# Kernel optimization log

Hardware: AMD Instinct MI355X
Metric: run time of the kernel (lower is better)

The kernel has to match this reference:

```python
import jax, jax.numpy as jnp
import numpy as np

BITS = 32
HDC_DIM = 512
IN_SCALE = 23  # 1 + 2*input_window_size, window=11


def setup_inputs() -> dict:
    key = jax.random.key(0)
    k1, k2, k3, k4 = jax.random.split(key, 4)
    B = 2
    D = IN_SCALE * IN_SCALE  # 529
    num_nonzero = int(0.5 * D * HDC_DIM)  # 135424
    return {
        "data_input": jax.random.normal(k1, (B, 4 * IN_SCALE, IN_SCALE), dtype=jnp.float32),
        "structure_input": jax.random.normal(k2, (B, IN_SCALE, IN_SCALE), dtype=jnp.float32),
        "parameters_temp": jax.random.uniform(k3, (IN_SCALE, IN_SCALE), dtype=jnp.float32),
        "non_zero_indices": jax.random.randint(k4, (num_nonzero,), 0, D * HDC_DIM, dtype=jnp.int32),
    }


def _bit_unpack(x_float):
    # view float32 bits as int32, unpack into 0/1 per bit (little-endian bit order),
    # matching torch: x.unsqueeze(-1).bitwise_and(2**arange(bits)).ne(0)
    xi = jax.lax.bitcast_convert_type(x_float, jnp.int32)
    mask = jnp.left_shift(jnp.int32(1), jnp.arange(BITS, dtype=jnp.int32))  # [32], incl. sign bit
    return ((xi[..., None] & mask) != 0).astype(jnp.int32)  # [..., 32]


def reference(data_input, structure_input, parameters_temp, non_zero_indices):
    B = data_input.shape[0]
    n = IN_SCALE
    # channel slices
    r = data_input[:, 0:n, :].reshape(B, -1)            # [B, D]
    g = data_input[:, n:2 * n, :].reshape(B, -1)
    b = data_input[:, 2 * n:3 * n, :].reshape(B, -1)
    a = data_input[:, 3 * n:4 * n, :].reshape(B, -1)
    s = (structure_input * parameters_temp).reshape(B, -1)  # [B, D]
    D = r.shape[1]

    # sparse random scatter into flat projection buffer (faithful to torch semantics:
    # view(-1)[idx] = 1, then view(-1)[~idx] = 0 where ~idx indexes total-1-idx via negative wrap)
    total = B * D * BITS * HDC_DIM
    proj = jnp.zeros((total,), dtype=jnp.int32)
    proj = proj.at[non_zero_indices].set(1)
    proj = proj.at[total - 1 - non_zero_indices].set(0)
    proj = proj.reshape(B, D, BITS, HDC_DIM)

    # bit-unpack + broadcast-XOR against projection (no materialized repeat)
    r_bin = _bit_unpack(r)[..., None] ^ proj  # [B, D, 32, hdc]
    g_bin = _bit_unpack(g)[..., None] ^ proj
    b_bin = _bit_unpack(b)[..., None] ^ proj
    a_bin = _bit_unpack(a)[..., None] ^ proj
    s_bin = _bit_unpack(s)[..., None] ^ proj

    return (r, g, b, a, s, r_bin, g_bin, b_bin, a_bin, s_bin)
```

## Files before the change

kernel.cpp:

```cpp
#include <hip/hip_runtime.h>
#include <stdint.h>

#define DDIM 529
#define BATCH 2
#define BITS 32
#define HDC 512
#define ROW (BITS * HDC)
#define NNZ_REGION (DDIM * HDC)
#define SMALL (5 * BATCH * DDIM)
#define BIN_PER_OUT (BATCH * DDIM * ROW)
#define TOTAL_FLOATS (SMALL + 5 * BIN_PER_OUT)
#define Q_BEG 1323
#define Q_END (TOTAL_FLOATS / 4)

typedef float f32x4 __attribute__((ext_vector_type(4)));

__device__ __forceinline__ unsigned rowword(int r,
                                            const float* __restrict__ data,
                                            const float* __restrict__ structure,
                                            const float* __restrict__ params) {
    int c   = r / (BATCH * DDIM);
    int rem = r - c * (BATCH * DDIM);
    int bb  = rem / DDIM;
    int d   = rem - bb * DDIM;
    float v = (c < 4) ? data[bb * (4 * DDIM) + c * DDIM + d]
                      : structure[bb * DDIM + d] * params[d];
    return (unsigned)__float_as_int(v);
}

__global__ __launch_bounds__(256) void stream4(const float* __restrict__ data,
                                               const float* __restrict__ structure,
                                               const float* __restrict__ params,
                                               float* __restrict__ out) {
    const unsigned nt = gridDim.x * 256u;
    f32x4* o4 = (f32x4*)out;
    for (unsigned q = Q_BEG + blockIdx.x * 256u + threadIdx.x; q < Q_END; q += nt) {
        unsigned E0 = 4u * q - SMALL;
        unsigned E2 = E0 + 2u;
        int r0 = (int)(E0 >> 14);
        int r2 = (int)(E2 >> 14);
        unsigned w0 = rowword(r0, data, structure, params);
        unsigned w2 = (r2 == r0) ? w0 : rowword(r2, data, structure, params);
        float fa = (float)((w0 >> ((E0 & 16383u) >> 9)) & 1u);
        float fb = (float)((w2 >> ((E2 & 16383u) >> 9)) & 1u);
        f32x4 v = {fa, fa, fb, fb};
        o4[q] = v;
    }
}

__global__ __launch_bounds__(256) void finalize(const int* __restrict__ idx, int n,
                                                const float* __restrict__ data,
                                                const float* __restrict__ structure,
                                                const float* __restrict__ params,
                                                float* __restrict__ out) {
    int i = blockIdx.x * blockDim.x + threadIdx.x;

    if (i < SMALL) {
        unsigned w = rowword(i, data, structure, params);
        out[i] = __int_as_float((int)w);
        if (i == 0) {
            float f = (float)(w & 1u);
            out[SMALL] = f; out[SMALL + 1] = f;
        }
        if (i == SMALL - 1) {
            float f = (float)(w >> 31);
            out[TOTAL_FLOATS - 2] = f; out[TOTAL_FLOATS - 1] = f;
        }
    }

    if (i < n) {
        unsigned p = (unsigned)idx[i];
        if (p < NNZ_REGION) {
            unsigned d = p >> 14;
            unsigned j = (p >> 9) & 31u;
            #pragma unroll
            for (int c = 0; c < 5; ++c) {
                float v = (c < 4) ? data[c * DDIM + d] : structure[d] * params[d];
                unsigned bit = ((unsigned)__float_as_int(v) >> j) & 1u;
                out[(size_t)SMALL + (size_t)c * BIN_PER_OUT + p] = (float)(bit ^ 1u);
            }
        }
    }
}

extern "C" void kernel_launch(void* const* d_in, const int* in_sizes, int n_in,
                              void* d_out, int out_size, void* d_ws, size_t ws_size,
                              hipStream_t stream) {
    const float* data      = (const float*)d_in[0];
    const float* structure = (const float*)d_in[1];
    const float* params    = (const float*)d_in[2];
    const int*   nzi       = (const int*)d_in[3];
    int nnz = in_sizes[3];

    float* out = (float*)d_out;

    stream4<<<2048, 256, 0, stream>>>(data, structure, params, out);
    finalize<<<(nnz + 255) / 256, 256, 0, stream>>>(nzi, nnz, data, structure, params, out);
}
```

Baseline: 83.81 us.

## Give each block a contiguous chunk and cache row words in shared memory

The streaming kernel now assigns each block a contiguous range of output quads instead of a grid-stride loop. The few source words that range needs are computed once into shared memory, which removes per-element global loads and integer divisions. The small-output writes and boundary fixups move from the finalize kernel into this prologue. The contiguous chunks give a different memory access pattern and add a block-wide barrier, and the hand-tuned chunk constants must exactly cover the output range.

Result: faster. 77.31 us (median of 2 runs) (-7.8%).

```diff
diff --git a/kernel.cpp b/kernel.cpp
--- a/kernel.cpp
+++ b/kernel.cpp
@@ -5,13 +5,14 @@
 #define BATCH 2
 #define BITS 32
 #define HDC 512
-#define ROW (BITS * HDC)
 #define NNZ_REGION (DDIM * HDC)
 #define SMALL (5 * BATCH * DDIM)
-#define BIN_PER_OUT (BATCH * DDIM * ROW)
+#define BIN_PER_OUT (BATCH * DDIM * 16384)
 #define TOTAL_FLOATS (SMALL + 5 * BIN_PER_OUT)
-#define Q_BEG 1323
+#define Q0 1328
 #define Q_END (TOTAL_FLOATS / 4)
+#define LQ 10584
+#define NBLK 2048
 
 typedef float f32x4 __attribute__((ext_vector_type(4)));
 
@@ -32,17 +33,39 @@
                                                const float* __restrict__ structure,
                                                const float* __restrict__ params,
                                                float* __restrict__ out) {
-    const unsigned nt = gridDim.x * 256u;
+    __shared__ int wds[4];
+    const unsigned qa = Q0 + blockIdx.x * LQ;
+    const unsigned qe = min(qa + LQ, (unsigned)Q_END);
+    const int r_lo = (int)((4u * qa - SMALL) >> 14);
+    const int t = threadIdx.x;
+    if (t < 4) {
+        int r = r_lo + t;
+        unsigned w = 0u;
+        if (r < SMALL) {
+            w = rowword(r, data, structure, params);
+            out[r] = __int_as_float((int)w);
+        }
+        wds[t] = (int)w;
+    } else if (blockIdx.x == 0) {
+        if (t >= 32 && t < 54) {
+            unsigned w0 = rowword(0, data, structure, params);
+            out[SMALL + (t - 32)] = (float)(w0 & 1u);
+        } else if (t == 54) {
+            unsigned w = rowword(SMALL - 1, data, structure, params);
+            float f = (float)(w >> 31);
+            out[TOTAL_FLOATS - 2] = f; out[TOTAL_FLOATS - 1] = f;
+        }
+    }
+    __syncthreads();
+
     f32x4* o4 = (f32x4*)out;
-    for (unsigned q = Q_BEG + blockIdx.x * 256u + threadIdx.x; q < Q_END; q += nt) {
+    for (unsigned q = qa + t; q < qe; q += 256u) {
         unsigned E0 = 4u * q - SMALL;
         unsigned E2 = E0 + 2u;
-        int r0 = (int)(E0 >> 14);
-        int r2 = (int)(E2 >> 14);
-        unsigned w0 = rowword(r0, data, structure, params);
-        unsigned w2 = (r2 == r0) ? w0 : rowword(r2, data, structure, params);
+        unsigned w0 = (unsigned)wds[(E0 >> 14) - r_lo];
+        unsigned w1 = (unsigned)wds[(E2 >> 14) - r_lo];
         float fa = (float)((w0 >> ((E0 & 16383u) >> 9)) & 1u);
-        float fb = (float)((w2 >> ((E2 & 16383u) >> 9)) & 1u);
+        float fb = (float)((w1 >> ((E2 & 16383u) >> 9)) & 1u);
         f32x4 v = {fa, fa, fb, fb};
         o4[q] = v;
     }
@@ -54,32 +77,16 @@
                                                 const float* __restrict__ params,
                                                 float* __restrict__ out) {
     int i = blockIdx.x * blockDim.x + threadIdx.x;
-
-    if (i < SMALL) {
-        unsigned w = rowword(i, data, structure, params);
-        out[i] = __int_as_float((int)w);
-        if (i == 0) {
-            float f = (float)(w & 1u);
-            out[SMALL] = f; out[SMALL + 1] = f;
-        }
-        if (i == SMALL - 1) {
-            float f = (float)(w >> 31);
-            out[TOTAL_FLOATS - 2] = f; out[TOTAL_FLOATS - 1] = f;
-        }
-    }
-
-    if (i < n) {
-        unsigned p = (unsigned)idx[i];
-        if (p < NNZ_REGION) {
-            unsigned d = p >> 14;
-            unsigned j = (p >> 9) & 31u;
-            #pragma unroll
-            for (int c = 0; c < 5; ++c) {
-                float v = (c < 4) ? data[c * DDIM + d] : structure[d] * params[d];
-                unsigned bit = ((unsigned)__float_as_int(v) >> j) & 1u;
-                out[(size_t)SMALL + (size_t)c * BIN_PER_OUT + p] = (float)(bit ^ 1u);
-            }
-        }
+    if (i >= n) return;
+    unsigned p = (unsigned)idx[i];
+    if (p >= NNZ_REGION) return;
+    unsigned d = p >> 14;
+    unsigned j = (p >> 9) & 31u;
+    #pragma unroll
+    for (int c = 0; c < 5; ++c) {
+        float v = (c < 4) ? data[c * DDIM + d] : structure[d] * params[d];
+        unsigned bit = ((unsigned)__float_as_int(v) >> j) & 1u;
+        out[(size_t)SMALL + (size_t)c * BIN_PER_OUT + p] = (float)(bit ^ 1u);
     }
 }
 
@@ -94,6 +101,6 @@
 
     float* out = (float*)d_out;
 
-    stream4<<<2048, 256, 0, stream>>>(data, structure, params, out);
+    stream4<<<NBLK, 256, 0, stream>>>(data, structure, params, out);
     finalize<<<(nnz + 255) / 256, 256, 0, stream>>>(nzi, nnz, data, structure, params, out);
 }
```
